# Performance work log

Hardware: AMD Instinct MI355X
Metric: run time of the kernel (lower is better)

The kernel has to match this reference:

```python
import math
import jax, jax.numpy as jnp
import numpy as np

TWO_PI = 2.0 * math.pi
LN_EPS = 1e-5


def wrap_angle(a):
    # wrap to (-pi, pi]
    return (a + math.pi) % TWO_PI - math.pi


def setup_inputs() -> dict:
    key = jax.random.key(0)
    ks = jax.random.split(key, 8)
    N = 2000          # num sources / targets (agents)
    E = 200000        # num edges
    D = 4             # input_dim (fixed by RelativeContextPositionEmbedding)
    NF = 64           # num_freq_bands
    H = 128           # hidden_dim
    F = 2 * NF + 1    # fourier feature width per input channel
    source = jax.random.normal(ks[0], (N, 3), jnp.float32)
    target = jax.random.normal(ks[1], (N, 5), jnp.float32)
    edge = jax.random.randint(ks[2], (2, E), 0, N, dtype=jnp.int32)
    freqs = jax.random.normal(ks[3], (D, NF), jnp.float32)          # nn.Embedding(D, NF).weight
    W1 = jax.random.normal(ks[4], (D, F, H), jnp.float32) * 0.02    # per-branch Linear1
    b1 = jnp.zeros((D, H), jnp.float32)
    gamma = jnp.ones((D, H), jnp.float32)                            # per-branch LayerNorm
    beta = jnp.zeros((D, H), jnp.float32)
    W2 = jax.random.normal(ks[5], (D, H, H), jnp.float32) * 0.02    # per-branch Linear2
    b2 = jnp.zeros((D, H), jnp.float32)
    return {"source": source, "target": target, "edge": edge, "freqs": freqs,
            "W1": W1, "b1": b1, "gamma": gamma, "beta": beta, "W2": W2, "b2": b2}


def _compute_feature(source, target, edge):
    src_pos, src_head = source[:, :2], source[:, 2]
    tgt_pos, tgt_head, tgt_speed = target[:, :2], target[:, 2], target[:, 3]
    e0, e1 = edge[0], edge[1]
    pd = src_pos[e0] - tgt_pos[e1]              # [E, 2]
    dx, dy = pd[:, 0], pd[:, 1]
    dh = wrap_angle(src_head[e0] - tgt_head[e1])
    ang = jnp.arctan2(dy, dx)
    tvx = tgt_speed * jnp.cos(tgt_head)
    tvy = tgt_speed * jnp.sin(tgt_head)
    closing = tvx[e1] * jnp.cos(ang) + tvy[e1] * jnp.sin(ang)
    return jnp.stack([dx, dy, dh, closing], axis=-1)  # [E, 4]


def reference(source, target, edge, freqs, W1, b1, gamma, beta, W2, b2):
    # feature computed under torch.no_grad() -> stop_gradient
    feat = jax.lax.stop_gradient(_compute_feature(source, target, edge))  # [E, D]
    x = feat[:, :, None] * freqs[None] * TWO_PI                            # [E, D, NF]
    x = jnp.concatenate([jnp.cos(x), jnp.sin(x), feat[:, :, None]], axis=-1)  # [E, D, F]
    # 4 small Linear -> LayerNorm -> ReLU -> Linear branches, vectorized over D
    h = jnp.einsum('edf,dfh->edh', x, W1) + b1                             # [E, D, H]
    mu = jnp.mean(h, axis=-1, keepdims=True)
    var = jnp.mean(jnp.square(h - mu), axis=-1, keepdims=True)
    h = (h - mu) * jax.lax.rsqrt(var + LN_EPS) * gamma + beta
    h = jax.nn.relu(h)
    y = jnp.einsum('edh,dhk->edk', h, W2) + b2                             # [E, D, H]
    return y.sum(axis=1)                                                   # [E, H]
```

## Files before the change

kernel.cpp:

```cpp
#include <hip/hip_runtime.h>
#include <hip/hip_bf16.h>
#include <math.h>

namespace {

typedef __attribute__((ext_vector_type(8))) short  short8;
typedef __attribute__((ext_vector_type(4))) float  float4v;

constexpr float PI_F     = 3.14159265358979323846f;
constexpr float TWO_PI_F = 6.28318530717958647692f;

__device__ __forceinline__ unsigned pack2(float a, float b) {
    __hip_bfloat162 h = __float22bfloat162_rn(float2{a, b});
    unsigned r;
    __builtin_memcpy(&r, &h, 4);
    return r;
}

union Frag { unsigned u[4]; short8 s; };

__device__ __forceinline__ void gl2lds16(const void* g, void* l) {
    __builtin_amdgcn_global_load_lds(
        (const __attribute__((address_space(1))) void*)g,
        (__attribute__((address_space(3))) void*)l, 16, 0, 0);
}

__device__ __forceinline__ void pb2() {
    asm volatile("s_waitcnt vmcnt(2) lgkmcnt(0)" ::: "memory");
    __builtin_amdgcn_s_barrier();
    __builtin_amdgcn_sched_barrier(0);
}
__device__ __forceinline__ void pb0() {
    asm volatile("s_waitcnt vmcnt(0) lgkmcnt(0)" ::: "memory");
    __builtin_amdgcn_s_barrier();
    __builtin_amdgcn_sched_barrier(0);
}

__device__ __forceinline__ void make_xf(const float* __restrict__ fq,
                                        float fe, int g, Frag* xf) {
    float cl[8], sl[8], ch8[8], sh8[8];
    #pragma unroll
    for (int j = 0; j < 8; ++j) {
        const float tL = fe * fq[8 * g + j];
        const float tH = fe * fq[32 + 8 * g + j];
        sl[j]  = __builtin_amdgcn_sinf(tL);
        cl[j]  = __builtin_amdgcn_cosf(tL);
        sh8[j] = __builtin_amdgcn_sinf(tH);
        ch8[j] = __builtin_amdgcn_cosf(tH);
    }
    #pragma unroll
    for (int p = 0; p < 4; ++p) {
        xf[0].u[p] = pack2(cl[2 * p],  cl[2 * p + 1]);
        xf[1].u[p] = pack2(ch8[2 * p], ch8[2 * p + 1]);
        xf[2].u[p] = pack2(sl[2 * p],  sl[2 * p + 1]);
        xf[3].u[p] = pack2(sh8[2 * p], sh8[2 * p + 1]);
    }
}

__global__ __launch_bounds__(256)
void prep_weights(const float* __restrict__ W1,
                  const float* __restrict__ W2,
                  ushort* __restrict__ W1T,
                  ushort* __restrict__ W2T) {
    const int idx = blockIdx.x * 256 + threadIdx.x;
    if (idx < 65536) {
        const int d = idx >> 14;
        const int n = (idx >> 7) & 127;
        const int k = idx & 127;
        __hip_bfloat16 v = __float2bfloat16(W1[(d * 129 + k) * 128 + n]);
        ushort u; __builtin_memcpy(&u, &v, 2);
        W1T[idx] = u;
    } else {
        const int j = idx - 65536;
        const int d = j >> 14;
        const int n = (j >> 7) & 127;
        const int kslot = j & 127;
        const int c = 32 * (kslot >> 5) + 16 * ((kslot >> 2) & 1)
                    + 4 * ((kslot >> 3) & 3) + (kslot & 3);
        __hip_bfloat16 v = __float2bfloat16(W2[(d * 128 + c) * 128 + n]);
        ushort u; __builtin_memcpy(&u, &v, 2);
        W2T[j] = u;
    }
}

__device__ __forceinline__ void stage_half(const ushort* __restrict__ Wtile,
                                           int half, ushort* slot, int wv, int lane) {
    const int e4 = lane & 15;
    const int g  = lane >> 4;
    #pragma unroll
    for (int i = 0; i < 2; ++i) {
        const int c  = 2 * wv + i;
        const int tt = c >> 2;
        const int ks = c & 3;
        const ushort* gp = Wtile + (16 * (4 * half + tt) + e4) * 128 + g * 8 + 32 * ks;
        gl2lds16(gp, slot + c * 512);
    }
}

__global__ __launch_bounds__(512, 4)
void rcpe_bal(const float* __restrict__ source,
              const float* __restrict__ target,
              const int*   __restrict__ edge,
              const float* __restrict__ freqs,
              const float* __restrict__ W1,
              const ushort* __restrict__ W1T,
              const float* __restrict__ b1,
              const float* __restrict__ gamma,
              const float* __restrict__ beta,
              const ushort* __restrict__ W2T,
              const float* __restrict__ b2,
              float* __restrict__ out,
              int E)
{
    __shared__ __align__(16) ushort wbuf[3][8192];
    __shared__ __align__(16) float b1_lds[4][128];
    __shared__ __align__(16) float gm_lds[4][128];
    __shared__ __align__(16) float bt_lds[4][128];
    __shared__ __align__(16) float w1r_lds[4][128];
    __shared__ __align__(16) float feat_lds[4][128];
    __shared__ __align__(16) float freq_lds[4][64];

    const int tid  = threadIdx.x;
    const int wv   = tid >> 6;
    const int lane = tid & 63;
    const int e4   = lane & 15;
    const int g    = lane >> 4;
    const int ebase = blockIdx.x * 128;
    const int eg    = ebase + wv * 16 + e4;

    stage_half(W1T, 0, wbuf[0], wv, lane);
    stage_half(W1T, 1, wbuf[1], wv, lane);
    __builtin_amdgcn_sched_barrier(0);

    {
        const int dd = tid >> 7, c = tid & 127;
        b1_lds[dd][c]  = b1[tid];
        gm_lds[dd][c]  = gamma[tid];
        bt_lds[dd][c]  = beta[tid];
        w1r_lds[dd][c] = W1[(dd * 129 + 128) * 128 + c];
    }
    if (tid < 256) ((float*)freq_lds)[tid] = freqs[tid];

    if (tid < 128) {
        const int e  = ebase + tid;
        const int ec = (e < E) ? e : (E - 1);
        const int s_i = edge[ec];
        const int t_i = edge[E + ec];
        const float sx = source[s_i * 3 + 0];
        const float sy = source[s_i * 3 + 1];
        const float sh = source[s_i * 3 + 2];
        const float tx = target[t_i * 5 + 0];
        const float ty = target[t_i * 5 + 1];
        const float th = target[t_i * 5 + 2];
        const float ts = target[t_i * 5 + 3];
        const float dx = sx - tx;
        const float dy = sy - ty;
        float a = sh - th + PI_F;
        a = fmodf(a, TWO_PI_F);
        if (a < 0.0f) a += TWO_PI_F;
        const float dh  = a - PI_F;
        const float ang = atan2f(dy, dx);
        const float tvx = ts * cosf(th);
        const float tvy = ts * sinf(th);
        const float closing = tvx * cosf(ang) + tvy * sinf(ang);
        feat_lds[0][tid] = dx;
        feat_lds[1][tid] = dy;
        feat_lds[2][tid] = dh;
        feat_lds[3][tid] = closing;
    }

    float4v y[8];
    #pragma unroll
    for (int t = 0; t < 8; ++t) {
        float4v a = {0.f, 0.f, 0.f, 0.f};
        #pragma unroll
        for (int d = 0; d < 4; ++d) {
            const float4v bv = *(const float4v*)(b2 + d * 128 + 16 * t + 4 * g);
            #pragma unroll
            for (int r = 0; r < 4; ++r) a[r] += bv[r];
        }
        y[t] = a;
    }

    pb2();

    float fe = feat_lds[0][wv * 16 + e4];
    Frag xf[4];
    make_xf(freq_lds[0], fe, g, xf);

    ushort* su  = wbuf[0];
    ushort* s1a = wbuf[1];
    ushort* s2a = wbuf[2];
    #define ROTATE() { ushort* _t = su; su = s1a; s1a = s2a; s2a = _t; }

    #pragma unroll 1
    for (int d = 0; d < 4; ++d) {
        stage_half(W2T + d * 16384, 0, s2a, wv, lane);

        float4v hacc[8];
        __builtin_amdgcn_s_setprio(1);
        #pragma unroll
        for (int t = 0; t < 4; ++t) {
            const float4v bv  = *(const float4v*)&b1_lds[d][16 * t + 4 * g];
            const float4v wr4 = *(const float4v*)&w1r_lds[d][16 * t + 4 * g];
            float4v acc;
            #pragma unroll
            for (int r = 0; r < 4; ++r) acc[r] = fmaf(fe, wr4[r], bv[r]);
            #pragma unroll
            for (int ks = 0; ks < 4; ++ks) {
                const short8 aw = *(const short8*)&su[(t * 4 + ks) * 512 + lane * 8];
                acc = __builtin_amdgcn_mfma_f32_16x16x32_bf16(aw, xf[ks].s, acc, 0, 0, 0);
            }
            hacc[t] = acc;
        }
        __builtin_amdgcn_s_setprio(0);
        pb2();
        ROTATE();

        stage_half(W2T + d * 16384, 1, s2a, wv, lane);

        __builtin_amdgcn_s_setprio(1);
        #pragma unroll
        for (int t = 4; t < 8; ++t) {
            const float4v bv  = *(const float4v*)&b1_lds[d][16 * t + 4 * g];
            const float4v wr4 = *(const float4v*)&w1r_lds[d][16 * t + 4 * g];
            float4v acc;
            #pragma unroll
            for (int r = 0; r < 4; ++r) acc[r] = fmaf(fe, wr4[r], bv[r]);
            #pragma unroll
            for (int ks = 0; ks < 4; ++ks) {
                const short8 aw = *(const short8*)&su[((t - 4) * 4 + ks) * 512 + lane * 8];
                acc = __builtin_amdgcn_mfma_f32_16x16x32_bf16(aw, xf[ks].s, acc, 0, 0, 0);
            }
            hacc[t] = acc;
        }
        __builtin_amdgcn_s_setprio(0);
        pb2();
        ROTATE();

        if (d < 3) stage_half(W1T + (d + 1) * 16384, 0, s2a, wv, lane);

        float sm = 0.f, sq = 0.f;
        #pragma unroll
        for (int t = 0; t < 8; ++t) {
            #pragma unroll
            for (int r = 0; r < 4; ++r) {
                const float v = hacc[t][r];
                sm += v;
                sq = fmaf(v, v, sq);
            }
        }
        sm += __shfl_xor(sm, 16, 64);
        sq += __shfl_xor(sq, 16, 64);
        sm += __shfl_xor(sm, 32, 64);
        sq += __shfl_xor(sq, 32, 64);
        const float mu   = sm * (1.f / 128.f);
        const float var  = sq * (1.f / 128.f) - mu * mu;
        const float rinv = rsqrtf(var + 1e-5f);
        #pragma unroll
        for (int t = 0; t < 8; ++t) {
            const float4v gv = *(const float4v*)&gm_lds[d][16 * t + 4 * g];
            const float4v bv = *(const float4v*)&bt_lds[d][16 * t + 4 * g];
            #pragma unroll
            for (int r = 0; r < 4; ++r) {
                float v = (hacc[t][r] - mu) * rinv;
                v = fmaf(v, gv[r], bv[r]);
                hacc[t][r] = fmaxf(v, 0.f);
            }
        }

        Frag bfr[4];
        #pragma unroll
        for (int ks = 0; ks < 4; ++ks) {
            bfr[ks].u[0] = pack2(hacc[2 * ks][0],     hacc[2 * ks][1]);
            bfr[ks].u[1] = pack2(hacc[2 * ks][2],     hacc[2 * ks][3]);
            bfr[ks].u[2] = pack2(hacc[2 * ks + 1][0], hacc[2 * ks + 1][1]);
            bfr[ks].u[3] = pack2(hacc[2 * ks + 1][2], hacc[2 * ks + 1][3]);
        }

        __builtin_amdgcn_s_setprio(1);
        #pragma unroll
        for (int t = 0; t < 4; ++t) {
            float4v acc = y[t];
            #pragma unroll
            for (int ks = 0; ks < 4; ++ks) {
                const short8 aw = *(const short8*)&su[(t * 4 + ks) * 512 + lane * 8];
                acc = __builtin_amdgcn_mfma_f32_16x16x32_bf16(aw, bfr[ks].s, acc, 0, 0, 0);
            }
            y[t] = acc;
        }
        __builtin_amdgcn_s_setprio(0);
        if (d < 3) pb2(); else pb0();
        ROTATE();

        if (d < 3) stage_half(W1T + (d + 1) * 16384, 1, s2a, wv, lane);

        __builtin_amdgcn_s_setprio(1);
        #pragma unroll
        for (int t = 4; t < 8; ++t) {
            float4v acc = y[t];
            #pragma unroll
            for (int ks = 0; ks < 4; ++ks) {
                const short8 aw = *(const short8*)&su[((t - 4) * 4 + ks) * 512 + lane * 8];
                acc = __builtin_amdgcn_mfma_f32_16x16x32_bf16(aw, bfr[ks].s, acc, 0, 0, 0);
            }
            y[t] = acc;
        }
        __builtin_amdgcn_s_setprio(0);

        if (d < 3) {
            fe = feat_lds[d + 1][wv * 16 + e4];
            make_xf(freq_lds[d + 1], fe, g, xf);
            pb2();
        }
        ROTATE();
    }
    #undef ROTATE

    if (eg < E) {
        #pragma unroll
        for (int t = 0; t < 8; ++t) {
            *(float4v*)(out + eg * 128 + 16 * t + 4 * g) = y[t];
        }
    }
}

}

extern "C" void kernel_launch(void* const* d_in, const int* in_sizes, int n_in,
                              void* d_out, int out_size, void* d_ws, size_t ws_size,
                              hipStream_t stream) {
    const float* source = (const float*)d_in[0];
    const float* target = (const float*)d_in[1];
    const int*   edge   = (const int*)  d_in[2];
    const float* freqs  = (const float*)d_in[3];
    const float* W1     = (const float*)d_in[4];
    const float* b1     = (const float*)d_in[5];
    const float* gammap = (const float*)d_in[6];
    const float* betap  = (const float*)d_in[7];
    const float* W2     = (const float*)d_in[8];
    const float* b2     = (const float*)d_in[9];
    float* out = (float*)d_out;

    ushort* W1T = (ushort*)d_ws;
    ushort* W2T = (ushort*)((char*)d_ws + 131072);

    const int E = in_sizes[2] / 2;

    prep_weights<<<dim3(512), dim3(256), 0, stream>>>(W1, W2, W1T, W2T);

    const int nblocks = (E + 127) / 128;
    rcpe_bal<<<dim3(nblocks), dim3(512), 0, stream>>>(
        source, target, edge, freqs, W1, W1T, b1, gammap, betap, W2T, b2, out, E);
}
```

Measured before the change: 112.4 us.

## Halve block size to 64 edges with double-buffered weight staging

Switches the kernel to 256-thread blocks each handling 64 edges, with two LDS weight buffers instead of three and plain __syncthreads barriers in place of partial vmcnt waits. Gamma and beta are packed into bf16 pairs to cut LDS footprint. The aim is more resident blocks and less LDS per block. In exchange, weights are restaged from global/L2 twice as often per edge, full barriers stall on outstanding loads, and gamma/beta lose precision. Bounds checks are removed, assuming E is a multiple of 64.

```diff
diff --git a/kernel.cpp b/kernel.cpp
--- a/kernel.cpp
+++ b/kernel.cpp
@@ -4,8 +4,9 @@
 
 namespace {
 
-typedef __attribute__((ext_vector_type(8))) short  short8;
-typedef __attribute__((ext_vector_type(4))) float  float4v;
+typedef __attribute__((ext_vector_type(8))) short    short8;
+typedef __attribute__((ext_vector_type(4))) float    float4v;
+typedef __attribute__((ext_vector_type(4))) unsigned uint4v;
 
 constexpr float PI_F     = 3.14159265358979323846f;
 constexpr float TWO_PI_F = 6.28318530717958647692f;
@@ -23,17 +24,6 @@
     __builtin_amdgcn_global_load_lds(
         (const __attribute__((address_space(1))) void*)g,
         (__attribute__((address_space(3))) void*)l, 16, 0, 0);
-}
-
-__device__ __forceinline__ void pb2() {
-    asm volatile("s_waitcnt vmcnt(2) lgkmcnt(0)" ::: "memory");
-    __builtin_amdgcn_s_barrier();
-    __builtin_amdgcn_sched_barrier(0);
-}
-__device__ __forceinline__ void pb0() {
-    asm volatile("s_waitcnt vmcnt(0) lgkmcnt(0)" ::: "memory");
-    __builtin_amdgcn_s_barrier();
-    __builtin_amdgcn_sched_barrier(0);
 }
 
 __device__ __forceinline__ void make_xf(const float* __restrict__ fq,
@@ -88,8 +78,8 @@
     const int e4 = lane & 15;
     const int g  = lane >> 4;
     #pragma unroll
-    for (int i = 0; i < 2; ++i) {
-        const int c  = 2 * wv + i;
+    for (int i = 0; i < 4; ++i) {
+        const int c  = 4 * wv + i;
         const int tt = c >> 2;
         const int ks = c & 3;
         const ushort* gp = Wtile + (16 * (4 * half + tt) + e4) * 128 + g * 8 + 32 * ks;
@@ -97,27 +87,26 @@
     }
 }
 
-__global__ __launch_bounds__(512, 4)
-void rcpe_bal(const float* __restrict__ source,
-              const float* __restrict__ target,
-              const int*   __restrict__ edge,
-              const float* __restrict__ freqs,
-              const float* __restrict__ W1,
-              const ushort* __restrict__ W1T,
-              const float* __restrict__ b1,
-              const float* __restrict__ gamma,
-              const float* __restrict__ beta,
-              const ushort* __restrict__ W2T,
-              const float* __restrict__ b2,
-              float* __restrict__ out,
-              int E)
+__global__ __launch_bounds__(256, 4)
+void rcpe_q(const float* __restrict__ source,
+            const float* __restrict__ target,
+            const int*   __restrict__ edge,
+            const float* __restrict__ freqs,
+            const float* __restrict__ W1,
+            const ushort* __restrict__ W1T,
+            const float* __restrict__ b1,
+            const float* __restrict__ gamma,
+            const float* __restrict__ beta,
+            const ushort* __restrict__ W2T,
+            const float* __restrict__ b2,
+            float* __restrict__ out,
+            int E)
 {
-    __shared__ __align__(16) ushort wbuf[3][8192];
+    __shared__ __align__(16) ushort wbuf[2][8192];
     __shared__ __align__(16) float b1_lds[4][128];
-    __shared__ __align__(16) float gm_lds[4][128];
-    __shared__ __align__(16) float bt_lds[4][128];
     __shared__ __align__(16) float w1r_lds[4][128];
-    __shared__ __align__(16) float feat_lds[4][128];
+    __shared__ __align__(16) unsigned gmbt_lds[4][128];
+    __shared__ __align__(16) float feat_lds[4][64];
     __shared__ __align__(16) float freq_lds[4][64];
 
     const int tid  = threadIdx.x;
@@ -125,27 +114,25 @@
     const int lane = tid & 63;
     const int e4   = lane & 15;
     const int g    = lane >> 4;
-    const int ebase = blockIdx.x * 128;
+    const int ebase = blockIdx.x * 64;
     const int eg    = ebase + wv * 16 + e4;
 
     stage_half(W1T, 0, wbuf[0], wv, lane);
-    stage_half(W1T, 1, wbuf[1], wv, lane);
-    __builtin_amdgcn_sched_barrier(0);
-
-    {
-        const int dd = tid >> 7, c = tid & 127;
-        b1_lds[dd][c]  = b1[tid];
-        gm_lds[dd][c]  = gamma[tid];
-        bt_lds[dd][c]  = beta[tid];
-        w1r_lds[dd][c] = W1[(dd * 129 + 128) * 128 + c];
-    }
-    if (tid < 256) ((float*)freq_lds)[tid] = freqs[tid];
-
-    if (tid < 128) {
-        const int e  = ebase + tid;
-        const int ec = (e < E) ? e : (E - 1);
-        const int s_i = edge[ec];
-        const int t_i = edge[E + ec];
+
+    #pragma unroll
+    for (int i = 0; i < 2; ++i) {
+        const int idx = tid + 256 * i;
+        const int dd = idx >> 7, c = idx & 127;
+        b1_lds[dd][c]   = b1[idx];
+        w1r_lds[dd][c]  = W1[(dd * 129 + 128) * 128 + c];
+        gmbt_lds[dd][c] = pack2(gamma[idx], beta[idx]);
+    }
+    ((float*)freq_lds)[tid] = freqs[tid];
+
+    if (tid < 64) {
+        const int e   = ebase + tid;
+        const int s_i = edge[e];
+        const int t_i = edge[E + e];
         const float sx = source[s_i * 3 + 0];
         const float sy = source[s_i * 3 + 1];
         const float sh = source[s_i * 3 + 2];
@@ -182,20 +169,19 @@
         y[t] = a;
     }
 
-    pb2();
+    __syncthreads();
 
     float fe = feat_lds[0][wv * 16 + e4];
     Frag xf[4];
     make_xf(freq_lds[0], fe, g, xf);
 
-    ushort* su  = wbuf[0];
-    ushort* s1a = wbuf[1];
-    ushort* s2a = wbuf[2];
-    #define ROTATE() { ushort* _t = su; su = s1a; s1a = s2a; s2a = _t; }
+    ushort* sA = wbuf[0];
+    ushort* sB = wbuf[1];
+    #define SWAP() { ushort* _t = sA; sA = sB; sB = _t; }
 
     #pragma unroll 1
     for (int d = 0; d < 4; ++d) {
-        stage_half(W2T + d * 16384, 0, s2a, wv, lane);
+        stage_half(W1T + d * 16384, 1, sB, wv, lane);
 
         float4v hacc[8];
         __builtin_amdgcn_s_setprio(1);
@@ -208,16 +194,16 @@
             for (int r = 0; r < 4; ++r) acc[r] = fmaf(fe, wr4[r], bv[r]);
             #pragma unroll
             for (int ks = 0; ks < 4; ++ks) {
-                const short8 aw = *(const short8*)&su[(t * 4 + ks) * 512 + lane * 8];
+                const short8 aw = *(const short8*)&sA[(t * 4 + ks) * 512 + lane * 8];
                 acc = __builtin_amdgcn_mfma_f32_16x16x32_bf16(aw, xf[ks].s, acc, 0, 0, 0);
             }
             hacc[t] = acc;
         }
         __builtin_amdgcn_s_setprio(0);
-        pb2();
-        ROTATE();
-
-        stage_half(W2T + d * 16384, 1, s2a, wv, lane);
+        __syncthreads();
+        SWAP();
+
+        stage_half(W2T + d * 16384, 0, sB, wv, lane);
 
         __builtin_amdgcn_s_setprio(1);
         #pragma unroll
@@ -229,16 +215,16 @@
             for (int r = 0; r < 4; ++r) acc[r] = fmaf(fe, wr4[r], bv[r]);
             #pragma unroll
             for (int ks = 0; ks < 4; ++ks) {
-                const short8 aw = *(const short8*)&su[((t - 4) * 4 + ks) * 512 + lane * 8];
+                const short8 aw = *(const short8*)&sA[((t - 4) * 4 + ks) * 512 + lane * 8];
                 acc = __builtin_amdgcn_mfma_f32_16x16x32_bf16(aw, xf[ks].s, acc, 0, 0, 0);
             }
             hacc[t] = acc;
         }
         __builtin_amdgcn_s_setprio(0);
-        pb2();
-        ROTATE();
-
-        if (d < 3) stage_half(W1T + (d + 1) * 16384, 0, s2a, wv, lane);
+        __syncthreads();
+        SWAP();
+
+        stage_half(W2T + d * 16384, 1, sB, wv, lane);
 
         float sm = 0.f, sq = 0.f;
         #pragma unroll
@@ -259,12 +245,13 @@
         const float rinv = rsqrtf(var + 1e-5f);
         #pragma unroll
         for (int t = 0; t < 8; ++t) {
-            const float4v gv = *(const float4v*)&gm_lds[d][16 * t + 4 * g];
-            const float4v bv = *(const float4v*)&bt_lds[d][16 * t + 4 * g];
+            const uint4v gb = *(const uint4v*)&gmbt_lds[d][16 * t + 4 * g];
             #pragma unroll
             for (int r = 0; r < 4; ++r) {
+                const float gv = __uint_as_float(gb[r] << 16);
+                const float bv = __uint_as_float(gb[r] & 0xFFFF0000u);
                 float v = (hacc[t][r] - mu) * rinv;
-                v = fmaf(v, gv[r], bv[r]);
+                v = fmaf(v, gv, bv);
                 hacc[t][r] = fmaxf(v, 0.f);
             }
         }
@@ -284,16 +271,16 @@
             float4v acc = y[t];
             #pragma unroll
             for (int ks = 0; ks < 4; ++ks) {
-                const short8 aw = *(const short8*)&su[(t * 4 + ks) * 512 + lane * 8];
+                const short8 aw = *(const short8*)&sA[(t * 4 + ks) * 512 + lane * 8];
                 acc = __builtin_amdgcn_mfma_f32_16x16x32_bf16(aw, bfr[ks].s, acc, 0, 0, 0);
             }
             y[t] = acc;
         }
         __builtin_amdgcn_s_setprio(0);
-        if (d < 3) pb2(); else pb0();
-        ROTATE();
-
-        if (d < 3) stage_half(W1T + (d + 1) * 16384, 1, s2a, wv, lane);
+        __syncthreads();
+        SWAP();
+
+        if (d < 3) stage_half(W1T + (d + 1) * 16384, 0, sB, wv, lane);
 
         __builtin_amdgcn_s_setprio(1);
         #pragma unroll
@@ -301,7 +288,7 @@
             float4v acc = y[t];
             #pragma unroll
             for (int ks = 0; ks < 4; ++ks) {
-                const short8 aw = *(const short8*)&su[((t - 4) * 4 + ks) * 512 + lane * 8];
+                const short8 aw = *(const short8*)&sA[((t - 4) * 4 + ks) * 512 + lane * 8];
                 acc = __builtin_amdgcn_mfma_f32_16x16x32_bf16(aw, bfr[ks].s, acc, 0, 0, 0);
             }
             y[t] = acc;
@@ -311,17 +298,15 @@
         if (d < 3) {
             fe = feat_lds[d + 1][wv * 16 + e4];
             make_xf(freq_lds[d + 1], fe, g, xf);
-            pb2();
-        }
-        ROTATE();
-    }
-    #undef ROTATE
-
-    if (eg < E) {
-        #pragma unroll
-        for (int t = 0; t < 8; ++t) {
-            *(float4v*)(out + eg * 128 + 16 * t + 4 * g) = y[t];
-        }
+            __syncthreads();
+        }
+        SWAP();
+    }
+    #undef SWAP
+
+    #pragma unroll
+    for (int t = 0; t < 8; ++t) {
+        *(float4v*)(out + eg * 128 + 16 * t + 4 * g) = y[t];
     }
 }
 
@@ -349,7 +334,7 @@
 
     prep_weights<<<dim3(512), dim3(256), 0, stream>>>(W1, W2, W1T, W2T);
 
-    const int nblocks = (E + 127) / 128;
-    rcpe_bal<<<dim3(nblocks), dim3(512), 0, stream>>>(
+    const int nblocks = E / 64;
+    rcpe_q<<<dim3(nblocks), dim3(256), 0, stream>>>(
         source, target, edge, freqs, W1, W1T, b1, gammap, betap, W2T, b2, out, E);
 }
```

New measurement: 137.1 us. 21.9% more time.
